# Performance work log

Measured on AMD Instinct MI355X. Metric: run time of the kernel, lower is better.

Reference implementation:

```python
import jax, jax.numpy as jnp
import numpy as np

WINDOW = 60
DEPTH = 3
HIDDEN = 256
LN_EPS = 1e-5


def _lyndon_indices(d):
    # Lyndon words over alphabet {0..d-1}, lengths 2 and 3, lexicographic order
    # (signatory mode='words' extracts expanded-logsig coefficients at Lyndon words).
    i2 = np.array([(i, j) for i in range(d) for j in range(d) if (i, j) < (j, i)], dtype=np.int32)
    i3 = np.array([(i, j, k) for i in range(d) for j in range(d) for k in range(d)
                   if (i, j, k) < (j, k, i) and (i, j, k) < (k, i, j)], dtype=np.int32)
    return i2, i3


def _logsig_features(x):
    # x: [b, s, c] -> logsignature of time-augmented sliding windows: [b*s, sig_channels]
    b, s, c = x.shape
    d = c + 1
    # replicate-padded sliding windows via clipped gather (matches F.pad replicate + unfold)
    pos = jnp.clip(jnp.arange(s)[:, None] + jnp.arange(WINDOW)[None, :] - (WINDOW - 1), 0, s - 1)
    windows = x[:, pos, :]                                   # [b, s, W, c]
    t = jnp.linspace(0.0, 1.0, WINDOW, dtype=x.dtype)        # time augmentation channel
    t_b = jnp.broadcast_to(t[None, None, :, None], (b, s, WINDOW, 1))
    aug = jnp.concatenate([t_b, windows], axis=-1).reshape(b * s, WINDOW, d)
    N = b * s
    # basepoint=True: prepend zero point -> increments include the first point itself
    inc = jnp.diff(aug, axis=1, prepend=jnp.zeros((N, 1, d), aug.dtype))  # [N, W, d]
    inc_t = jnp.transpose(inc, (1, 0, 2))                    # [W, N, d]

    def chen_step(carry, v):
        S1, S2, S3 = carry
        vv = jnp.einsum('ni,nj->nij', v, v)
        vvv = jnp.einsum('nij,nk->nijk', vv, v)
        nS3 = S3 + jnp.einsum('nij,nk->nijk', S2, v) \
                 + 0.5 * jnp.einsum('ni,njk->nijk', S1, vv) + vvv / 6.0
        nS2 = S2 + jnp.einsum('ni,nj->nij', S1, v) + 0.5 * vv
        nS1 = S1 + v
        return (nS1, nS2, nS3), None

    init = (jnp.zeros((N, d), x.dtype), jnp.zeros((N, d, d), x.dtype), jnp.zeros((N, d, d, d), x.dtype))
    (S1, S2, S3), _ = jax.lax.scan(chen_step, init, inc_t)
    # log in truncated tensor algebra: log(1+x) = x - x^2/2 + x^3/3
    L1 = S1
    L2 = S2 - 0.5 * jnp.einsum('ni,nj->nij', S1, S1)
    L3 = (S3 - 0.5 * (jnp.einsum('ni,njk->nijk', S1, S2) + jnp.einsum('nij,nk->nijk', S2, S1))
          + jnp.einsum('ni,nj,nk->nijk', S1, S1, S1) / 3.0)
    i2, i3 = _lyndon_indices(d)
    f2 = L2[:, i2[:, 0], i2[:, 1]]
    f3 = L3[:, i3[:, 0], i3[:, 1], i3[:, 2]]
    return jnp.concatenate([L1, f2, f3], axis=-1)            # [N, sig_channels]


def setup_inputs() -> dict:
    key = jax.random.key(0)
    ks = jax.random.split(key, 5)
    b, s, c = 8, 2048, 8
    d = c + 1
    sig_channels = d + (d * d - d) // 2 + (d ** 3 - d) // 3  # 285 for d=9
    h2 = 2 * HIDDEN
    x = jax.random.normal(ks[0], (b, s, c), dtype=jnp.float32)
    w1 = jax.random.normal(ks[1], (sig_channels, h2), dtype=jnp.float32) / np.sqrt(sig_channels)
    b1 = jnp.zeros((h2,), jnp.float32)
    ln_g = jnp.ones((h2,), jnp.float32)
    ln_b = jnp.zeros((h2,), jnp.float32)
    w2 = jax.random.normal(ks[2], (h2, HIDDEN), dtype=jnp.float32) / np.sqrt(h2)
    b2 = jnp.zeros((HIDDEN,), jnp.float32)
    return {"x": x, "w1": w1, "b1": b1, "ln_g": ln_g, "ln_b": ln_b, "w2": w2, "b2": b2}


def reference(x, w1, b1, ln_g, ln_b, w2, b2):
    b, s, _ = x.shape
    feats = _logsig_features(x)                              # [b*s, sig_channels]
    h = jax.nn.gelu(feats @ w1 + b1, approximate=False)      # torch default GELU (erf)
    mu = jnp.mean(h, axis=-1, keepdims=True)
    var = jnp.var(h, axis=-1, keepdims=True)
    h = (h - mu) / jnp.sqrt(var + LN_EPS) * ln_g + ln_b      # LayerNorm; Dropout is eval no-op
    out = h @ w2 + b2
    return out.reshape(b, s, -1)
```

## Files before the change

### kernel.cpp

```cpp
#include <hip/hip_runtime.h>
#include <hip/hip_bf16.h>
#include <cstdint>
#include <cstddef>

typedef short short8 __attribute__((ext_vector_type(8)));
typedef float f32x4 __attribute__((ext_vector_type(4)));
typedef float f32x2 __attribute__((ext_vector_type(2)));

#define NS    2048
#define KPAD  288
#define H2    512
#define HID   256
#define WPB   7
#define SBLK  293

#define MFMA(a,b,c) __builtin_amdgcn_mfma_f32_16x16x32_bf16((a),(b),(c),0,0,0)

__device__ __forceinline__ void gl2lds16(const void* g, void* l) {
    __builtin_amdgcn_global_load_lds(
        (const __attribute__((address_space(1))) void*)g,
        (__attribute__((address_space(3))) void*)l, 16, 0, 0);
}
__device__ __forceinline__ float geluf(float x) {
    return 0.5f * x * (1.0f + erff(x * 0.70710678118654752f));
}
__device__ __forceinline__ f32x4 shfl4(f32x4 v, int d) {
    f32x4 r;
    r[0] = __shfl_xor(v[0], d); r[1] = __shfl_xor(v[1], d);
    r[2] = __shfl_xor(v[2], d); r[3] = __shfl_xor(v[3], d);
    return r;
}

struct Tbl3 { short col[729]; };
static constexpr Tbl3 make_tbl3() {
    Tbl3 t{};
    for (int x = 0; x < 729; ++x) t.col[x] = -1;
    int r = 0;
    for (int i = 0; i < 9; ++i)
        for (int j = 0; j < 9; ++j)
            for (int k = 0; k < 9; ++k) {
                bool lt1 = (i < j) || (i == j && (j < k || (j == k && k < i)));
                bool lt2 = (i < k) || (i == k && (j < i || (j == i && k < j)));
                if (lt1 && lt2) { t.col[(i*9+j)*9+k] = (short)(45 + r); ++r; }
            }
    return t;
}
static constexpr Tbl3 TBL3 = make_tbl3();

#define SIG_STEP(VA_,VB_,VC_) { \
    const float hh = 0.5f * S1i + vi * (1.0f/6.0f); \
    const float ra = S2ra + hh * (VA_); \
    const float rb = S2rb + hh * (VB_); \
    const float rc = S2rc + hh * (VC_); \
    const f32x2 ra2 = {ra, ra}, rb2 = {rb, rb}, rc2 = {rc, rc}; \
    S3sa += ra * v0; S3pa0 += ra2*vp0; S3pa1 += ra2*vp1; S3pa2 += ra2*vp2; S3pa3 += ra2*vp3; \
    S3sb += rb * v0; S3pb0 += rb2*vp0; S3pb1 += rb2*vp1; S3pb2 += rb2*vp2; S3pb3 += rb2*vp3; \
    S3sc += rc * v0; S3pc0 += rc2*vp0; S3pc1 += rc2*vp1; S3pc2 += rc2*vp2; S3pc3 += rc2*vp3; \
    const float aa = S1i + 0.5f * vi; \
    S2ra += aa * (VA_); S2rb += aa * (VB_); S2rc += aa * (VC_); \
    S1i += vi; }

#define SIG_MAIN(VA_,VB_,VC_) { \
    { const float* xr = &X[(g0 - lo) * 8]; \
      const float4 e0 = *(const float4*)xr; \
      const float4 e1 = *(const float4*)(xr + 4); \
      const float rs = xr[ioff]; \
      const float v0 = 0.0f; \
      const f32x2 vp0 = {e0.x, e0.y}, vp1 = {e0.z, e0.w}, vp2 = {e1.x, e1.y}, vp3 = {e1.z, e1.w}; \
      const float vi = (ci == 0) ? 0.0f : rs; \
      SIG_STEP(VA_,VB_,VC_) } \
    const float* pd = &PD[(sm59 + 1 - lo + 59) * 8]; \
    float4 d0 = *(const float4*)pd; \
    float4 d1 = *(const float4*)(pd + 4); \
    float rn = pd[ioff]; \
    _Pragma("unroll 2") \
    for (int j = 1; j < 60; ++j) { \
      const float4 e0 = d0; const float4 e1 = d1; const float rs = rn; \
      pd += 8; \
      d0 = *(const float4*)pd; d1 = *(const float4*)(pd + 4); rn = pd[ioff]; \
      const float v0 = DT; \
      const f32x2 vp0 = {e0.x, e0.y}, vp1 = {e0.z, e0.w}, vp2 = {e1.x, e1.y}, vp3 = {e1.z, e1.w}; \
      const float vi = (ci == 0) ? DT : rs; \
      SIG_STEP(VA_,VB_,VC_) \
    } }

#define SIG_ST(RA,RB,RC) \
    if (act) { \
        if ((RA) == 0) S1buf[widx * 9 + ci] = S1i; \
        float* sb = &S2buf[widx * 81 + ci * 9]; \
        sb[RA] = S2ra; sb[RB] = S2rb; sb[RC] = S2rc; \
    }

#define S3EL0(SL) S3s##SL
#define S3EL1(SL) S3p##SL##0[0]
#define S3EL2(SL) S3p##SL##0[1]
#define S3EL3(SL) S3p##SL##1[0]
#define S3EL4(SL) S3p##SL##1[1]
#define S3EL5(SL) S3p##SL##2[0]
#define S3EL6(SL) S3p##SL##2[1]
#define S3EL7(SL) S3p##SL##3[0]
#define S3EL8(SL) S3p##SL##3[1]

#define SIG_E2(SL,J2) if (ci < (J2)) { \
    const float val2 = S2r##SL - 0.5f * S1i * s1v##J2; \
    const int col2 = 9 + ci*8 - (ci*(ci-1))/2 + ((J2) - ci - 1); \
    frow[col2] = __float2bfloat16(val2); }

#define SIG_E3(SL,R,K) { const int col3 = TBL3.col[tb + (R)*9 + (K)]; \
    if (col3 >= 0) { \
        const float val3 = S3EL##K(SL) \
            - 0.5f * (S1i * S2w[(R)*9+(K)] + S2r##SL * s1v##K) \
            + S1i * s1v##R * s1v##K * (1.0f/3.0f); \
        frow[col3] = __float2bfloat16(val3); } }

#define SIG_E3R(SL,R) SIG_E3(SL,R,0) SIG_E3(SL,R,1) SIG_E3(SL,R,2) SIG_E3(SL,R,3) \
    SIG_E3(SL,R,4) SIG_E3(SL,R,5) SIG_E3(SL,R,6) SIG_E3(SL,R,7) SIG_E3(SL,R,8)

#define SIG_EMIT(RA,RB,RC) \
    if (act) { \
        if ((RA) == 0) { \
            frow[ci] = __float2bfloat16(S1i); \
            if (ci == 0) { \
                const __hip_bfloat16 z16 = __float2bfloat16(0.0f); \
                frow[285] = z16; frow[286] = z16; frow[287] = z16; \
            } \
        } \
        SIG_E2(a,RA) SIG_E2(b,RB) SIG_E2(c,RC) \
        SIG_E3R(a,RA) SIG_E3R(b,RB) SIG_E3R(c,RC) \
    }

__global__ __launch_bounds__(192) __attribute__((amdgpu_waves_per_eu(1, 6)))
void sig_kernel(const float* __restrict__ x, __hip_bfloat16* __restrict__ feats) {
    __shared__ __align__(16) float X[66 * 8];
    __shared__ __align__(16) float PD[126 * 8];
    __shared__ float S2buf[WPB * 81];
    __shared__ float S1buf[WPB * 9];

    const int blk = blockIdx.x;
    const int b   = blk / SBLK;
    const int s0  = (blk % SBLK) * WPB;
    const int lo  = (s0 - 59 > 0) ? (s0 - 59) : 0;
    const int hi  = (s0 + WPB - 1 < NS - 1) ? (s0 + WPB - 1) : (NS - 1);
    const int nrow = hi - lo + 1;
    const int tid = threadIdx.x;

    {
        const float4* src = (const float4*)(x + ((size_t)b * NS + lo) * 8);
        float4* X4 = (float4*)X;
        const int n4 = nrow * 2;
        for (int t = tid; t < n4; t += 192) X4[t] = src[t];
    }
    __syncthreads();
    {
        const float4* X4 = (const float4*)X;
        float4* PD4 = (float4*)PD;
        for (int t = tid; t < 252; t += 192) {
            const int p = t >> 1;
            const int r = p - 59;
            float4 dv = {0.f, 0.f, 0.f, 0.f};
            if (r > 0 && r < nrow) {
                const float4 a = X4[t - 118], bb = X4[t - 120];
                dv.x = a.x - bb.x; dv.y = a.y - bb.y; dv.z = a.z - bb.z; dv.w = a.w - bb.w;
            }
            PD4[t] = dv;
        }
    }
    __syncthreads();

    const int t3    = tid >> 6;
    const int lt    = tid & 63;
    const int widx0 = lt / 9;
    const int ci    = lt - widx0 * 9;
    const bool act  = (lt < 63) && (s0 + widx0 < NS);
    const int widx  = (widx0 < WPB - 1) ? widx0 : WPB - 1;
    int s = s0 + widx; if (s > NS - 1) s = NS - 1;

    float S3sa=0.f, S3sb=0.f, S3sc=0.f;
    f32x2 S3pa0={0.f,0.f},S3pa1={0.f,0.f},S3pa2={0.f,0.f},S3pa3={0.f,0.f};
    f32x2 S3pb0={0.f,0.f},S3pb1={0.f,0.f},S3pb2={0.f,0.f},S3pb3={0.f,0.f};
    f32x2 S3pc0={0.f,0.f},S3pc1={0.f,0.f},S3pc2={0.f,0.f},S3pc3={0.f,0.f};
    float S2ra=0.f, S2rb=0.f, S2rc=0.f;
    float S1i = 0.f;
    const int ioff = (ci > 0) ? (ci - 1) : 0;
    const int sm59 = s - 59;
    const int g0   = (sm59 > 0) ? sm59 : 0;
    const float DT = 1.0f / 59.0f;

    if (t3 == 0)      { SIG_MAIN(v0,   e0.x, e0.y) }
    else if (t3 == 1) { SIG_MAIN(e0.z, e0.w, e1.x) }
    else              { SIG_MAIN(e1.y, e1.z, e1.w) }

    if (t3 == 0)      { SIG_ST(0,1,2) }
    else if (t3 == 1) { SIG_ST(3,4,5) }
    else              { SIG_ST(6,7,8) }
    __syncthreads();

    const float* s1p = &S1buf[widx * 9];
    const float s1v0=s1p[0], s1v1=s1p[1], s1v2=s1p[2], s1v3=s1p[3], s1v4=s1p[4];
    const float s1v5=s1p[5], s1v6=s1p[6], s1v7=s1p[7], s1v8=s1p[8];
    const float* S2w = &S2buf[widx * 81];
    const int tb = ci * 81;
    __hip_bfloat16* frow = feats + (size_t)(b * NS + s) * KPAD;

    if (t3 == 0)      { SIG_EMIT(0,1,2) }
    else if (t3 == 1) { SIG_EMIT(3,4,5) }
    else              { SIG_EMIT(6,7,8) }
}

__global__ void convert_w1(const float* __restrict__ w1, __hip_bfloat16* __restrict__ w1T) {
    const int n = blockIdx.x;
    const int k = threadIdx.x;
    const float v = (k < 285) ? w1[(size_t)k * H2 + n] : 0.0f;
    w1T[(size_t)n * KPAD + k] = __float2bfloat16(v);
}
__global__ void convert_w2g(const float* __restrict__ w2, const float* __restrict__ lng,
                            const float* __restrict__ lnb, const float* __restrict__ b2,
                            __hip_bfloat16* __restrict__ w2g, float* __restrict__ gw,
                            float* __restrict__ cvec) {
    const int n = blockIdx.x, k = threadIdx.x;
    const float wv = w2[(size_t)k * HID + n];
    const float a = lng[k] * wv;
    const float c = lnb[k] * wv;
    w2g[(size_t)n * H2 + k] = __float2bfloat16(a);
    float ra = a, rc = c;
#pragma unroll
    for (int d = 1; d < 64; d <<= 1) { ra += __shfl_xor(ra, d); rc += __shfl_xor(rc, d); }
    __shared__ float r1[8], r2[8];
    const int wv_ = k >> 6, ln = k & 63;
    if (ln == 0) { r1[wv_] = ra; r2[wv_] = rc; }
    __syncthreads();
    if (k == 0) {
        float sa = 0.f, sc = 0.f;
#pragma unroll
        for (int i = 0; i < 8; ++i) { sa += r1[i]; sc += r2[i]; }
        gw[n] = sa; cvec[n] = sc + b2[n];
    }
}

#define GDECL \
    f32x4 acc00={0,0,0,0},acc01={0,0,0,0},acc02={0,0,0,0},acc03={0,0,0,0}; \
    f32x4 acc10={0,0,0,0},acc11={0,0,0,0},acc12={0,0,0,0},acc13={0,0,0,0}; \
    f32x4 acc20={0,0,0,0},acc21={0,0,0,0},acc22={0,0,0,0},acc23={0,0,0,0}; \
    f32x4 acc30={0,0,0,0},acc31={0,0,0,0},acc32={0,0,0,0},acc33={0,0,0,0};

#define GMROW(mf) { const short8 av = *(const short8*)(abase + (mf)*512); \
    acc##mf##0 = MFMA(av, b0v, acc##mf##0); acc##mf##1 = MFMA(av, b1v, acc##mf##1); \
    acc##mf##2 = MFMA(av, b2v, acc##mf##2); acc##mf##3 = MFMA(av, b3v, acc##mf##3); }

#define GEMM_KLOOP(APTR, BPTR, KD, KSTEPS) \
    _Pragma("unroll 1") \
    for (int kt = 0; kt < (KSTEPS); ++kt) { \
        const int K0 = kt * 32; \
        { int c = tid; \
          gl2lds16((APTR) + (size_t)(m0 + (c>>2))*(KD) + K0 + (c&3)*8, (char*)ldsA + (c & ~63)*16); \
          gl2lds16((BPTR) + (size_t)(n0 + (c>>2))*(KD) + K0 + (c&3)*8, (char*)ldsB + (c & ~63)*16); \
          c = tid + 256; \
          gl2lds16((APTR) + (size_t)(m0 + (c>>2))*(KD) + K0 + (c&3)*8, (char*)ldsA + (c & ~63)*16); \
          gl2lds16((BPTR) + (size_t)(n0 + (c>>2))*(KD) + K0 + (c&3)*8, (char*)ldsB + (c & ~63)*16); } \
        __syncthreads(); \
        const __hip_bfloat16* abase = ldsA + (mh + l16)*32 + quad*8; \
        const __hip_bfloat16* bbase = ldsB + (nh + l16)*32 + quad*8; \
        const short8 b0v = *(const short8*)(bbase); \
        const short8 b1v = *(const short8*)(bbase + 512); \
        const short8 b2v = *(const short8*)(bbase + 1024); \
        const short8 b3v = *(const short8*)(bbase + 1536); \
        GMROW(0) GMROW(1) GMROW(2) GMROW(3) \
        __syncthreads(); \
    }

#define G1EP(mf,nf) { \
    const int colv = n0 + nh + (nf)*16 + l16; \
    const float bv = bias[colv]; \
    f32x4 e; \
    e[0] = geluf(acc##mf##nf[0] + bv); e[1] = geluf(acc##mf##nf[1] + bv); \
    e[2] = geluf(acc##mf##nf[2] + bv); e[3] = geluf(acc##mf##nf[3] + bv); \
    const int rrow = m0 + mh + (mf)*16 + quad*4; \
    h1[(size_t)(rrow+0)*H2 + colv] = __float2bfloat16(e[0]); \
    h1[(size_t)(rrow+1)*H2 + colv] = __float2bfloat16(e[1]); \
    h1[(size_t)(rrow+2)*H2 + colv] = __float2bfloat16(e[2]); \
    h1[(size_t)(rrow+3)*H2 + colv] = __float2bfloat16(e[3]); \
    sum##mf += e; sq##mf += e*e; }

#define G1RED(mf) { \
    f32x4 s = sum##mf, q = sq##mf; \
    s += shfl4(s,1); q += shfl4(q,1); s += shfl4(s,2); q += shfl4(q,2); \
    s += shfl4(s,4); q += shfl4(q,4); s += shfl4(s,8); q += shfl4(q,8); \
    if (l16 == 0) { const int rrow = m0 + mh + (mf)*16 + quad*4; \
        atomicAdd(&stats[2*(rrow+0)],   s[0]); atomicAdd(&stats[2*(rrow+0)+1], q[0]); \
        atomicAdd(&stats[2*(rrow+1)],   s[1]); atomicAdd(&stats[2*(rrow+1)+1], q[1]); \
        atomicAdd(&stats[2*(rrow+2)],   s[2]); atomicAdd(&stats[2*(rrow+2)+1], q[2]); \
        atomicAdd(&stats[2*(rrow+3)],   s[3]); atomicAdd(&stats[2*(rrow+3)+1], q[3]); } }

__global__ __launch_bounds__(256) __attribute__((amdgpu_waves_per_eu(1, 4)))
void gemm1_kernel(const __hip_bfloat16* __restrict__ feats,
                  const __hip_bfloat16* __restrict__ w1T,
                  const float* __restrict__ bias,
                  __hip_bfloat16* __restrict__ h1,
                  float* __restrict__ stats) {
    __shared__ __align__(16) __hip_bfloat16 ldsA[128 * 32];
    __shared__ __align__(16) __hip_bfloat16 ldsB[128 * 32];
    const int tid  = threadIdx.x;
    const int wave = tid >> 6;
    const int lane = tid & 63;
    const int quad = lane >> 4;
    const int l16  = lane & 15;
    const int mh   = (wave >> 1) * 64;
    const int nh   = (wave & 1) * 64;
    const int m0   = blockIdx.x * 128;
    const int n0   = blockIdx.y * 128;
    GDECL
    GEMM_KLOOP(feats, w1T, KPAD, 9)
    f32x4 sum0={0,0,0,0},sum1={0,0,0,0},sum2={0,0,0,0},sum3={0,0,0,0};
    f32x4 sq0={0,0,0,0},sq1={0,0,0,0},sq2={0,0,0,0},sq3={0,0,0,0};
    G1EP(0,0) G1EP(0,1) G1EP(0,2) G1EP(0,3)
    G1EP(1,0) G1EP(1,1) G1EP(1,2) G1EP(1,3)
    G1EP(2,0) G1EP(2,1) G1EP(2,2) G1EP(2,3)
    G1EP(3,0) G1EP(3,1) G1EP(3,2) G1EP(3,3)
    G1RED(0) G1RED(1) G1RED(2) G1RED(3)
}

#define STATR(r) { const float su = stats[2*(rrow+(r))]; const float qu = stats[2*(rrow+(r))+1]; \
    const float m_ = su * (1.0f/512.0f); const float v_ = qu * (1.0f/512.0f) - m_*m_; \
    muv[r] = m_; rsv[r] = rsqrtf(v_ + 1e-5f); }

#define G2C(mf,nf) { const int colv = n0 + nh + (nf)*16 + l16; \
    const float g_ = gw[colv], c_ = cvec[colv]; \
    out[(size_t)(rrow+0)*HID + colv] = rsv[0]*(acc##mf##nf[0] - muv[0]*g_) + c_; \
    out[(size_t)(rrow+1)*HID + colv] = rsv[1]*(acc##mf##nf[1] - muv[1]*g_) + c_; \
    out[(size_t)(rrow+2)*HID + colv] = rsv[2]*(acc##mf##nf[2] - muv[2]*g_) + c_; \
    out[(size_t)(rrow+3)*HID + colv] = rsv[3]*(acc##mf##nf[3] - muv[3]*g_) + c_; }

#define G2EP(mf) { const int rrow = m0 + mh + (mf)*16 + quad*4; \
    f32x4 muv, rsv; \
    STATR(0) STATR(1) STATR(2) STATR(3) \
    G2C(mf,0) G2C(mf,1) G2C(mf,2) G2C(mf,3) }

__global__ __launch_bounds__(256) __attribute__((amdgpu_waves_per_eu(1, 4)))
void gemm2_kernel(const __hip_bfloat16* __restrict__ h1,
                  const __hip_bfloat16* __restrict__ w2g,
                  const float* __restrict__ stats,
                  const float* __restrict__ gw,
                  const float* __restrict__ cvec,
                  float* __restrict__ out) {
    __shared__ __align__(16) __hip_bfloat16 ldsA[128 * 32];
    __shared__ __align__(16) __hip_bfloat16 ldsB[128 * 32];
    const int tid  = threadIdx.x;
    const int wave = tid >> 6;
    const int lane = tid & 63;
    const int quad = lane >> 4;
    const int l16  = lane & 15;
    const int mh   = (wave >> 1) * 64;
    const int nh   = (wave & 1) * 64;
    const int m0   = blockIdx.x * 128;
    const int n0   = blockIdx.y * 128;
    GDECL
    GEMM_KLOOP(h1, w2g, H2, 16)
    G2EP(0) G2EP(1) G2EP(2) G2EP(3)
}

extern "C" void kernel_launch(void* const* d_in, const int* in_sizes, int n_in,
                              void* d_out, int out_size, void* d_ws, size_t ws_size,
                              hipStream_t stream) {
    const float* x   = (const float*)d_in[0];
    const float* w1  = (const float*)d_in[1];
    const float* b1  = (const float*)d_in[2];
    const float* lng = (const float*)d_in[3];
    const float* lnb = (const float*)d_in[4];
    const float* w2  = (const float*)d_in[5];
    const float* b2  = (const float*)d_in[6];
    float* out = (float*)d_out;

    char* ws = (char*)d_ws;
    __hip_bfloat16* feats = (__hip_bfloat16*)(ws);
    __hip_bfloat16* h1    = (__hip_bfloat16*)(ws + 9437184);
    __hip_bfloat16* w1T   = (__hip_bfloat16*)(ws + 26214400);
    __hip_bfloat16* w2g   = (__hip_bfloat16*)(ws + 26509312);
    float*          gw    = (float*)(ws + 26771456);
    float*          cvec  = (float*)(ws + 26775552);
    float*          stats = (float*)(ws + 26779648);

    hipMemsetAsync(stats, 0, 16384 * 2 * sizeof(float), stream);
    convert_w1<<<dim3(512), dim3(288), 0, stream>>>(w1, w1T);
    convert_w2g<<<dim3(256), dim3(512), 0, stream>>>(w2, lng, lnb, b2, w2g, gw, cvec);
    sig_kernel<<<dim3(8 * SBLK), dim3(192), 0, stream>>>(x, feats);
    gemm1_kernel<<<dim3(128, 4), dim3(256), 0, stream>>>(feats, w1T, b1, h1, stats);
    gemm2_kernel<<<dim3(128, 2), dim3(256), 0, stream>>>(h1, w2g, stats, gw, cvec, out);
}
```

Baseline: 163.7 us.

## Fuse LayerNorm into GEMM1 with full-row tiles and direct-register MFMA loads

GEMM1 now gives each block 64 full rows of all 512 hidden columns, so the LayerNorm statistics can be reduced in shared memory and applied in the epilogue. This removes the global atomic stats buffer, its memset, and the folded gamma/beta weights used by GEMM2. Both GEMMs drop LDS staging and load MFMA operands straight from global memory into registers. GEMM2 becomes a plain GEMM plus bias with smaller 32-row tiles. The trade-off is more register pressure from 16 accumulators per wave and no LDS reuse of the B tiles, which now depends on L1/L2 caching.

New measurement: 204.7 us. 25.1% more time.

```diff
diff --git a/kernel.cpp b/kernel.cpp
--- a/kernel.cpp
+++ b/kernel.cpp
@@ -16,11 +16,6 @@
 
 #define MFMA(a,b,c) __builtin_amdgcn_mfma_f32_16x16x32_bf16((a),(b),(c),0,0,0)
 
-__device__ __forceinline__ void gl2lds16(const void* g, void* l) {
-    __builtin_amdgcn_global_load_lds(
-        (const __attribute__((address_space(1))) void*)g,
-        (__attribute__((address_space(3))) void*)l, 16, 0, 0);
-}
 __device__ __forceinline__ float geluf(float x) {
     return 0.5f * x * (1.0f + erff(x * 0.70710678118654752f));
 }
@@ -213,149 +208,131 @@
     const float v = (k < 285) ? w1[(size_t)k * H2 + n] : 0.0f;
     w1T[(size_t)n * KPAD + k] = __float2bfloat16(v);
 }
-__global__ void convert_w2g(const float* __restrict__ w2, const float* __restrict__ lng,
-                            const float* __restrict__ lnb, const float* __restrict__ b2,
-                            __hip_bfloat16* __restrict__ w2g, float* __restrict__ gw,
-                            float* __restrict__ cvec) {
-    const int n = blockIdx.x, k = threadIdx.x;
-    const float wv = w2[(size_t)k * HID + n];
-    const float a = lng[k] * wv;
-    const float c = lnb[k] * wv;
-    w2g[(size_t)n * H2 + k] = __float2bfloat16(a);
-    float ra = a, rc = c;
-#pragma unroll
-    for (int d = 1; d < 64; d <<= 1) { ra += __shfl_xor(ra, d); rc += __shfl_xor(rc, d); }
-    __shared__ float r1[8], r2[8];
-    const int wv_ = k >> 6, ln = k & 63;
-    if (ln == 0) { r1[wv_] = ra; r2[wv_] = rc; }
-    __syncthreads();
-    if (k == 0) {
-        float sa = 0.f, sc = 0.f;
-#pragma unroll
-        for (int i = 0; i < 8; ++i) { sa += r1[i]; sc += r2[i]; }
-        gw[n] = sa; cvec[n] = sc + b2[n];
-    }
-}
-
-#define GDECL \
-    f32x4 acc00={0,0,0,0},acc01={0,0,0,0},acc02={0,0,0,0},acc03={0,0,0,0}; \
-    f32x4 acc10={0,0,0,0},acc11={0,0,0,0},acc12={0,0,0,0},acc13={0,0,0,0}; \
-    f32x4 acc20={0,0,0,0},acc21={0,0,0,0},acc22={0,0,0,0},acc23={0,0,0,0}; \
-    f32x4 acc30={0,0,0,0},acc31={0,0,0,0},acc32={0,0,0,0},acc33={0,0,0,0};
-
-#define GMROW(mf) { const short8 av = *(const short8*)(abase + (mf)*512); \
-    acc##mf##0 = MFMA(av, b0v, acc##mf##0); acc##mf##1 = MFMA(av, b1v, acc##mf##1); \
-    acc##mf##2 = MFMA(av, b2v, acc##mf##2); acc##mf##3 = MFMA(av, b3v, acc##mf##3); }
-
-#define GEMM_KLOOP(APTR, BPTR, KD, KSTEPS) \
-    _Pragma("unroll 1") \
-    for (int kt = 0; kt < (KSTEPS); ++kt) { \
-        const int K0 = kt * 32; \
-        { int c = tid; \
-          gl2lds16((APTR) + (size_t)(m0 + (c>>2))*(KD) + K0 + (c&3)*8, (char*)ldsA + (c & ~63)*16); \
-          gl2lds16((BPTR) + (size_t)(n0 + (c>>2))*(KD) + K0 + (c&3)*8, (char*)ldsB + (c & ~63)*16); \
-          c = tid + 256; \
-          gl2lds16((APTR) + (size_t)(m0 + (c>>2))*(KD) + K0 + (c&3)*8, (char*)ldsA + (c & ~63)*16); \
-          gl2lds16((BPTR) + (size_t)(n0 + (c>>2))*(KD) + K0 + (c&3)*8, (char*)ldsB + (c & ~63)*16); } \
-        __syncthreads(); \
-        const __hip_bfloat16* abase = ldsA + (mh + l16)*32 + quad*8; \
-        const __hip_bfloat16* bbase = ldsB + (nh + l16)*32 + quad*8; \
-        const short8 b0v = *(const short8*)(bbase); \
-        const short8 b1v = *(const short8*)(bbase + 512); \
-        const short8 b2v = *(const short8*)(bbase + 1024); \
-        const short8 b3v = *(const short8*)(bbase + 1536); \
-        GMROW(0) GMROW(1) GMROW(2) GMROW(3) \
-        __syncthreads(); \
-    }
-
-#define G1EP(mf,nf) { \
-    const int colv = n0 + nh + (nf)*16 + l16; \
-    const float bv = bias[colv]; \
-    f32x4 e; \
-    e[0] = geluf(acc##mf##nf[0] + bv); e[1] = geluf(acc##mf##nf[1] + bv); \
-    e[2] = geluf(acc##mf##nf[2] + bv); e[3] = geluf(acc##mf##nf[3] + bv); \
-    const int rrow = m0 + mh + (mf)*16 + quad*4; \
-    h1[(size_t)(rrow+0)*H2 + colv] = __float2bfloat16(e[0]); \
-    h1[(size_t)(rrow+1)*H2 + colv] = __float2bfloat16(e[1]); \
-    h1[(size_t)(rrow+2)*H2 + colv] = __float2bfloat16(e[2]); \
-    h1[(size_t)(rrow+3)*H2 + colv] = __float2bfloat16(e[3]); \
-    sum##mf += e; sq##mf += e*e; }
-
-#define G1RED(mf) { \
-    f32x4 s = sum##mf, q = sq##mf; \
-    s += shfl4(s,1); q += shfl4(q,1); s += shfl4(s,2); q += shfl4(q,2); \
-    s += shfl4(s,4); q += shfl4(q,4); s += shfl4(s,8); q += shfl4(q,8); \
-    if (l16 == 0) { const int rrow = m0 + mh + (mf)*16 + quad*4; \
-        atomicAdd(&stats[2*(rrow+0)],   s[0]); atomicAdd(&stats[2*(rrow+0)+1], q[0]); \
-        atomicAdd(&stats[2*(rrow+1)],   s[1]); atomicAdd(&stats[2*(rrow+1)+1], q[1]); \
-        atomicAdd(&stats[2*(rrow+2)],   s[2]); atomicAdd(&stats[2*(rrow+2)+1], q[2]); \
-        atomicAdd(&stats[2*(rrow+3)],   s[3]); atomicAdd(&stats[2*(rrow+3)+1], q[3]); } }
-
-__global__ __launch_bounds__(256) __attribute__((amdgpu_waves_per_eu(1, 4)))
+__global__ void convert_w2(const float* __restrict__ w2, __hip_bfloat16* __restrict__ w2T) {
+    const int n = blockIdx.x;
+    const int k = threadIdx.x;
+    w2T[(size_t)n * H2 + k] = __float2bfloat16(w2[(size_t)k * HID + n]);
+}
+
+#define REP16(M) M(0) M(1) M(2) M(3) M(4) M(5) M(6) M(7) M(8) M(9) M(10) M(11) M(12) M(13) M(14) M(15)
+#define REP8(M)  M(0) M(1) M(2) M(3) M(4) M(5) M(6) M(7)
+
+#define G1_DECL(nf) f32x4 acc##nf = {0.f,0.f,0.f,0.f};
+#define G1_LD(nf)   const short8 bv##nf = *(const short8*)(brow + (nf)*16*KPAD + ko);
+#define G1_FM(nf)   acc##nf = MFMA(av, bv##nf, acc##nf);
+#define G1_BIAS(nf) const float bias##nf = b1[wc*256 + (nf)*16 + l16];
+#define G1_GELU(nf) { acc##nf[0]=geluf(acc##nf[0]+bias##nf); acc##nf[1]=geluf(acc##nf[1]+bias##nf); \
+                      acc##nf[2]=geluf(acc##nf[2]+bias##nf); acc##nf[3]=geluf(acc##nf[3]+bias##nf); }
+#define G1_OUT(nf) { const int col = wc*256 + (nf)*16 + l16; \
+    const float g_ = lng[col], b_ = lnb[col]; \
+    hp[0*H2 + col] = __float2bfloat16((acc##nf[0]-mu0)*rs0*g_ + b_); \
+    hp[1*H2 + col] = __float2bfloat16((acc##nf[1]-mu1)*rs1*g_ + b_); \
+    hp[2*H2 + col] = __float2bfloat16((acc##nf[2]-mu2)*rs2*g_ + b_); \
+    hp[3*H2 + col] = __float2bfloat16((acc##nf[3]-mu3)*rs3*g_ + b_); }
+
+__global__ __launch_bounds__(512) __attribute__((amdgpu_waves_per_eu(1, 4)))
 void gemm1_kernel(const __hip_bfloat16* __restrict__ feats,
                   const __hip_bfloat16* __restrict__ w1T,
-                  const float* __restrict__ bias,
-                  __hip_bfloat16* __restrict__ h1,
-                  float* __restrict__ stats) {
-    __shared__ __align__(16) __hip_bfloat16 ldsA[128 * 32];
-    __shared__ __align__(16) __hip_bfloat16 ldsB[128 * 32];
+                  const float* __restrict__ b1,
+                  const float* __restrict__ lng,
+                  const float* __restrict__ lnb,
+                  __hip_bfloat16* __restrict__ h1) {
+    __shared__ float lnpart[2][64][2];
+    __shared__ float lnstat[64][2];
     const int tid  = threadIdx.x;
     const int wave = tid >> 6;
     const int lane = tid & 63;
     const int quad = lane >> 4;
     const int l16  = lane & 15;
-    const int mh   = (wave >> 1) * 64;
-    const int nh   = (wave & 1) * 64;
-    const int m0   = blockIdx.x * 128;
-    const int n0   = blockIdx.y * 128;
-    GDECL
-    GEMM_KLOOP(feats, w1T, KPAD, 9)
-    f32x4 sum0={0,0,0,0},sum1={0,0,0,0},sum2={0,0,0,0},sum3={0,0,0,0};
-    f32x4 sq0={0,0,0,0},sq1={0,0,0,0},sq2={0,0,0,0},sq3={0,0,0,0};
-    G1EP(0,0) G1EP(0,1) G1EP(0,2) G1EP(0,3)
-    G1EP(1,0) G1EP(1,1) G1EP(1,2) G1EP(1,3)
-    G1EP(2,0) G1EP(2,1) G1EP(2,2) G1EP(2,3)
-    G1EP(3,0) G1EP(3,1) G1EP(3,2) G1EP(3,3)
-    G1RED(0) G1RED(1) G1RED(2) G1RED(3)
-}
-
-#define STATR(r) { const float su = stats[2*(rrow+(r))]; const float qu = stats[2*(rrow+(r))+1]; \
-    const float m_ = su * (1.0f/512.0f); const float v_ = qu * (1.0f/512.0f) - m_*m_; \
-    muv[r] = m_; rsv[r] = rsqrtf(v_ + 1e-5f); }
-
-#define G2C(mf,nf) { const int colv = n0 + nh + (nf)*16 + l16; \
-    const float g_ = gw[colv], c_ = cvec[colv]; \
-    out[(size_t)(rrow+0)*HID + colv] = rsv[0]*(acc##mf##nf[0] - muv[0]*g_) + c_; \
-    out[(size_t)(rrow+1)*HID + colv] = rsv[1]*(acc##mf##nf[1] - muv[1]*g_) + c_; \
-    out[(size_t)(rrow+2)*HID + colv] = rsv[2]*(acc##mf##nf[2] - muv[2]*g_) + c_; \
-    out[(size_t)(rrow+3)*HID + colv] = rsv[3]*(acc##mf##nf[3] - muv[3]*g_) + c_; }
-
-#define G2EP(mf) { const int rrow = m0 + mh + (mf)*16 + quad*4; \
-    f32x4 muv, rsv; \
-    STATR(0) STATR(1) STATR(2) STATR(3) \
-    G2C(mf,0) G2C(mf,1) G2C(mf,2) G2C(mf,3) }
+    const int wr   = wave >> 1;
+    const int wc   = wave & 1;
+    const int m0   = blockIdx.x * 64;
+
+    const __hip_bfloat16* arow = feats + (size_t)(m0 + wr*16 + l16) * KPAD + quad*8;
+    const __hip_bfloat16* brow = w1T   + (size_t)(wc*256 + l16) * KPAD + quad*8;
+
+    REP16(G1_DECL)
+#pragma unroll 1
+    for (int kt = 0; kt < 9; ++kt) {
+        const int ko = kt * 32;
+        const short8 av = *(const short8*)(arow + ko);
+        REP16(G1_LD)
+        REP16(G1_FM)
+    }
+
+    REP16(G1_BIAS)
+    REP16(G1_GELU)
+
+    f32x4 s = acc0+acc1+acc2+acc3+acc4+acc5+acc6+acc7+acc8+acc9+acc10+acc11+acc12+acc13+acc14+acc15;
+    f32x4 q = acc0*acc0+acc1*acc1+acc2*acc2+acc3*acc3+acc4*acc4+acc5*acc5+acc6*acc6+acc7*acc7
+            + acc8*acc8+acc9*acc9+acc10*acc10+acc11*acc11+acc12*acc12+acc13*acc13+acc14*acc14+acc15*acc15;
+    s += shfl4(s,1); q += shfl4(q,1);
+    s += shfl4(s,2); q += shfl4(q,2);
+    s += shfl4(s,4); q += shfl4(q,4);
+    s += shfl4(s,8); q += shfl4(q,8);
+    if (l16 == 0) {
+#pragma unroll
+        for (int r = 0; r < 4; ++r) {
+            lnpart[wc][wr*16 + quad*4 + r][0] = s[r];
+            lnpart[wc][wr*16 + quad*4 + r][1] = q[r];
+        }
+    }
+    __syncthreads();
+    if (tid < 64) {
+        const float su = lnpart[0][tid][0] + lnpart[1][tid][0];
+        const float qu = lnpart[0][tid][1] + lnpart[1][tid][1];
+        const float mu  = su * (1.0f / 512.0f);
+        const float var = qu * (1.0f / 512.0f) - mu * mu;
+        lnstat[tid][0] = mu;
+        lnstat[tid][1] = rsqrtf(var + 1e-5f);
+    }
+    __syncthreads();
+    const int rb = wr*16 + quad*4;
+    const float mu0 = lnstat[rb+0][0], rs0 = lnstat[rb+0][1];
+    const float mu1 = lnstat[rb+1][0], rs1 = lnstat[rb+1][1];
+    const float mu2 = lnstat[rb+2][0], rs2 = lnstat[rb+2][1];
+    const float mu3 = lnstat[rb+3][0], rs3 = lnstat[rb+3][1];
+    __hip_bfloat16* hp = h1 + (size_t)(m0 + rb) * H2;
+    REP16(G1_OUT)
+}
+
+#define G2_DECL(nf) f32x4 acc##nf = {0.f,0.f,0.f,0.f};
+#define G2_LD(nf)   const short8 bv##nf = *(const short8*)(brow + (nf)*16*H2 + ko);
+#define G2_FM(nf)   acc##nf = MFMA(av, bv##nf, acc##nf);
+#define G2_OUT(nf) { const int col = wc*128 + (nf)*16 + l16; \
+    const float b_ = b2[col]; \
+    op[0*HID + col] = acc##nf[0] + b_; \
+    op[1*HID + col] = acc##nf[1] + b_; \
+    op[2*HID + col] = acc##nf[2] + b_; \
+    op[3*HID + col] = acc##nf[3] + b_; }
 
 __global__ __launch_bounds__(256) __attribute__((amdgpu_waves_per_eu(1, 4)))
 void gemm2_kernel(const __hip_bfloat16* __restrict__ h1,
-                  const __hip_bfloat16* __restrict__ w2g,
-                  const float* __restrict__ stats,
-                  const float* __restrict__ gw,
-                  const float* __restrict__ cvec,
+                  const __hip_bfloat16* __restrict__ w2T,
+                  const float* __restrict__ b2,
                   float* __restrict__ out) {
-    __shared__ __align__(16) __hip_bfloat16 ldsA[128 * 32];
-    __shared__ __align__(16) __hip_bfloat16 ldsB[128 * 32];
     const int tid  = threadIdx.x;
     const int wave = tid >> 6;
     const int lane = tid & 63;
     const int quad = lane >> 4;
     const int l16  = lane & 15;
-    const int mh   = (wave >> 1) * 64;
-    const int nh   = (wave & 1) * 64;
-    const int m0   = blockIdx.x * 128;
-    const int n0   = blockIdx.y * 128;
-    GDECL
-    GEMM_KLOOP(h1, w2g, H2, 16)
-    G2EP(0) G2EP(1) G2EP(2) G2EP(3)
+    const int wr   = wave >> 1;
+    const int wc   = wave & 1;
+    const int m0   = blockIdx.x * 32;
+
+    const __hip_bfloat16* arow = h1  + (size_t)(m0 + wr*16 + l16) * H2 + quad*8;
+    const __hip_bfloat16* brow = w2T + (size_t)(wc*128 + l16) * H2 + quad*8;
+
+    REP8(G2_DECL)
+#pragma unroll 1
+    for (int kt = 0; kt < 16; ++kt) {
+        const int ko = kt * 32;
+        const short8 av = *(const short8*)(arow + ko);
+        REP8(G2_LD)
+        REP8(G2_FM)
+    }
+    float* op = out + (size_t)(m0 + wr*16 + quad*4) * HID;
+    REP8(G2_OUT)
 }
 
 extern "C" void kernel_launch(void* const* d_in, const int* in_sizes, int n_in,
@@ -374,15 +351,11 @@
     __hip_bfloat16* feats = (__hip_bfloat16*)(ws);
     __hip_bfloat16* h1    = (__hip_bfloat16*)(ws + 9437184);
     __hip_bfloat16* w1T   = (__hip_bfloat16*)(ws + 26214400);
-    __hip_bfloat16* w2g   = (__hip_bfloat16*)(ws + 26509312);
-    float*          gw    = (float*)(ws + 26771456);
-    float*          cvec  = (float*)(ws + 26775552);
-    float*          stats = (float*)(ws + 26779648);
-
-    hipMemsetAsync(stats, 0, 16384 * 2 * sizeof(float), stream);
+    __hip_bfloat16* w2T   = (__hip_bfloat16*)(ws + 26509312);
+
     convert_w1<<<dim3(512), dim3(288), 0, stream>>>(w1, w1T);
-    convert_w2g<<<dim3(256), dim3(512), 0, stream>>>(w2, lng, lnb, b2, w2g, gw, cvec);
+    convert_w2<<<dim3(256), dim3(512), 0, stream>>>(w2, w2T);
     sig_kernel<<<dim3(8 * SBLK), dim3(192), 0, stream>>>(x, feats);
-    gemm1_kernel<<<dim3(128, 4), dim3(256), 0, stream>>>(feats, w1T, b1, h1, stats);
-    gemm2_kernel<<<dim3(128, 2), dim3(256), 0, stream>>>(h1, w2g, stats, gw, cvec, out);
-}
+    gemm1_kernel<<<dim3(16384 / 64), dim3(512), 0, stream>>>(feats, w1T, b1, lng, lnb, h1);
+    gemm2_kernel<<<dim3(16384 / 32), dim3(256), 0, stream>>>(h1, w2T, b2, out);
+}
```

## Keep full-K weight slice in LDS, stream A from global, drop atomics

Applied to the files above, without the earlier changes.

Both GEMMs are retiled so each block loads its whole-K slice of the weight matrix into padded LDS once. Each wave then streams its 32 A rows straight from global memory with no per-k-step barriers, and the grid grows to 128x8 blocks. LayerNorm row statistics are written as per-column-block partials into a 16-slot layout and summed in gemm2, replacing the atomics and the memset. The trade-off is less A reuse per block, more redundant A traffic across column blocks, and unpipelined global loads feeding the MFMAs.

New measurement: 167.1 us. +2.1%, slower.

```diff
diff --git a/kernel.cpp b/kernel.cpp
--- a/kernel.cpp
+++ b/kernel.cpp
@@ -13,14 +13,11 @@
 #define HID   256
 #define WPB   7
 #define SBLK  293
+#define KLDS1 296
+#define KLDS2 520
 
 #define MFMA(a,b,c) __builtin_amdgcn_mfma_f32_16x16x32_bf16((a),(b),(c),0,0,0)
 
-__device__ __forceinline__ void gl2lds16(const void* g, void* l) {
-    __builtin_amdgcn_global_load_lds(
-        (const __attribute__((address_space(1))) void*)g,
-        (__attribute__((address_space(3))) void*)l, 16, 0, 0);
-}
 __device__ __forceinline__ float geluf(float x) {
     return 0.5f * x * (1.0f + erff(x * 0.70710678118654752f));
 }
@@ -237,103 +234,97 @@
     }
 }
 
-#define GDECL \
-    f32x4 acc00={0,0,0,0},acc01={0,0,0,0},acc02={0,0,0,0},acc03={0,0,0,0}; \
-    f32x4 acc10={0,0,0,0},acc11={0,0,0,0},acc12={0,0,0,0},acc13={0,0,0,0}; \
-    f32x4 acc20={0,0,0,0},acc21={0,0,0,0},acc22={0,0,0,0},acc23={0,0,0,0}; \
-    f32x4 acc30={0,0,0,0},acc31={0,0,0,0},acc32={0,0,0,0},acc33={0,0,0,0};
-
-#define GMROW(mf) { const short8 av = *(const short8*)(abase + (mf)*512); \
-    acc##mf##0 = MFMA(av, b0v, acc##mf##0); acc##mf##1 = MFMA(av, b1v, acc##mf##1); \
-    acc##mf##2 = MFMA(av, b2v, acc##mf##2); acc##mf##3 = MFMA(av, b3v, acc##mf##3); }
-
-#define GEMM_KLOOP(APTR, BPTR, KD, KSTEPS) \
-    _Pragma("unroll 1") \
-    for (int kt = 0; kt < (KSTEPS); ++kt) { \
-        const int K0 = kt * 32; \
-        { int c = tid; \
-          gl2lds16((APTR) + (size_t)(m0 + (c>>2))*(KD) + K0 + (c&3)*8, (char*)ldsA + (c & ~63)*16); \
-          gl2lds16((BPTR) + (size_t)(n0 + (c>>2))*(KD) + K0 + (c&3)*8, (char*)ldsB + (c & ~63)*16); \
-          c = tid + 256; \
-          gl2lds16((APTR) + (size_t)(m0 + (c>>2))*(KD) + K0 + (c&3)*8, (char*)ldsA + (c & ~63)*16); \
-          gl2lds16((BPTR) + (size_t)(n0 + (c>>2))*(KD) + K0 + (c&3)*8, (char*)ldsB + (c & ~63)*16); } \
-        __syncthreads(); \
-        const __hip_bfloat16* abase = ldsA + (mh + l16)*32 + quad*8; \
-        const __hip_bfloat16* bbase = ldsB + (nh + l16)*32 + quad*8; \
-        const short8 b0v = *(const short8*)(bbase); \
-        const short8 b1v = *(const short8*)(bbase + 512); \
-        const short8 b2v = *(const short8*)(bbase + 1024); \
-        const short8 b3v = *(const short8*)(bbase + 1536); \
-        GMROW(0) GMROW(1) GMROW(2) GMROW(3) \
-        __syncthreads(); \
-    }
-
-#define G1EP(mf,nf) { \
-    const int colv = n0 + nh + (nf)*16 + l16; \
-    const float bv = bias[colv]; \
-    f32x4 e; \
-    e[0] = geluf(acc##mf##nf[0] + bv); e[1] = geluf(acc##mf##nf[1] + bv); \
-    e[2] = geluf(acc##mf##nf[2] + bv); e[3] = geluf(acc##mf##nf[3] + bv); \
-    const int rrow = m0 + mh + (mf)*16 + quad*4; \
-    h1[(size_t)(rrow+0)*H2 + colv] = __float2bfloat16(e[0]); \
-    h1[(size_t)(rrow+1)*H2 + colv] = __float2bfloat16(e[1]); \
-    h1[(size_t)(rrow+2)*H2 + colv] = __float2bfloat16(e[2]); \
-    h1[(size_t)(rrow+3)*H2 + colv] = __float2bfloat16(e[3]); \
-    sum##mf += e; sq##mf += e*e; }
-
-#define G1RED(mf) { \
-    f32x4 s = sum##mf, q = sq##mf; \
-    s += shfl4(s,1); q += shfl4(q,1); s += shfl4(s,2); q += shfl4(q,2); \
-    s += shfl4(s,4); q += shfl4(q,4); s += shfl4(s,8); q += shfl4(q,8); \
-    if (l16 == 0) { const int rrow = m0 + mh + (mf)*16 + quad*4; \
-        atomicAdd(&stats[2*(rrow+0)],   s[0]); atomicAdd(&stats[2*(rrow+0)+1], q[0]); \
-        atomicAdd(&stats[2*(rrow+1)],   s[1]); atomicAdd(&stats[2*(rrow+1)+1], q[1]); \
-        atomicAdd(&stats[2*(rrow+2)],   s[2]); atomicAdd(&stats[2*(rrow+2)+1], q[2]); \
-        atomicAdd(&stats[2*(rrow+3)],   s[3]); atomicAdd(&stats[2*(rrow+3)+1], q[3]); } }
-
 __global__ __launch_bounds__(256) __attribute__((amdgpu_waves_per_eu(1, 4)))
 void gemm1_kernel(const __hip_bfloat16* __restrict__ feats,
                   const __hip_bfloat16* __restrict__ w1T,
-                  const float* __restrict__ bias,
+                  const float* __restrict__ b1,
                   __hip_bfloat16* __restrict__ h1,
                   float* __restrict__ stats) {
-    __shared__ __align__(16) __hip_bfloat16 ldsA[128 * 32];
-    __shared__ __align__(16) __hip_bfloat16 ldsB[128 * 32];
+    __shared__ __align__(16) __hip_bfloat16 ldsB[64 * KLDS1];
     const int tid  = threadIdx.x;
     const int wave = tid >> 6;
     const int lane = tid & 63;
     const int quad = lane >> 4;
     const int l16  = lane & 15;
-    const int mh   = (wave >> 1) * 64;
-    const int nh   = (wave & 1) * 64;
-    const int m0   = blockIdx.x * 128;
-    const int n0   = blockIdx.y * 128;
-    GDECL
-    GEMM_KLOOP(feats, w1T, KPAD, 9)
-    f32x4 sum0={0,0,0,0},sum1={0,0,0,0},sum2={0,0,0,0},sum3={0,0,0,0};
-    f32x4 sq0={0,0,0,0},sq1={0,0,0,0},sq2={0,0,0,0},sq3={0,0,0,0};
-    G1EP(0,0) G1EP(0,1) G1EP(0,2) G1EP(0,3)
-    G1EP(1,0) G1EP(1,1) G1EP(1,2) G1EP(1,3)
-    G1EP(2,0) G1EP(2,1) G1EP(2,2) G1EP(2,3)
-    G1EP(3,0) G1EP(3,1) G1EP(3,2) G1EP(3,3)
-    G1RED(0) G1RED(1) G1RED(2) G1RED(3)
-}
-
-#define STATR(r) { const float su = stats[2*(rrow+(r))]; const float qu = stats[2*(rrow+(r))+1]; \
-    const float m_ = su * (1.0f/512.0f); const float v_ = qu * (1.0f/512.0f) - m_*m_; \
-    muv[r] = m_; rsv[r] = rsqrtf(v_ + 1e-5f); }
-
-#define G2C(mf,nf) { const int colv = n0 + nh + (nf)*16 + l16; \
-    const float g_ = gw[colv], c_ = cvec[colv]; \
-    out[(size_t)(rrow+0)*HID + colv] = rsv[0]*(acc##mf##nf[0] - muv[0]*g_) + c_; \
-    out[(size_t)(rrow+1)*HID + colv] = rsv[1]*(acc##mf##nf[1] - muv[1]*g_) + c_; \
-    out[(size_t)(rrow+2)*HID + colv] = rsv[2]*(acc##mf##nf[2] - muv[2]*g_) + c_; \
-    out[(size_t)(rrow+3)*HID + colv] = rsv[3]*(acc##mf##nf[3] - muv[3]*g_) + c_; }
-
-#define G2EP(mf) { const int rrow = m0 + mh + (mf)*16 + quad*4; \
-    f32x4 muv, rsv; \
-    STATR(0) STATR(1) STATR(2) STATR(3) \
-    G2C(mf,0) G2C(mf,1) G2C(mf,2) G2C(mf,3) }
+    const int m0   = blockIdx.x * 128 + wave * 32;
+    const int n0   = blockIdx.y * 64;
+    const int nb   = blockIdx.y;
+
+    for (int c = tid; c < 64 * 36; c += 256) {
+        const int n = c / 36, k8 = c - n * 36;
+        *(short8*)(ldsB + n * KLDS1 + k8 * 8) =
+            *(const short8*)(w1T + (size_t)(n0 + n) * KPAD + k8 * 8);
+    }
+    __syncthreads();
+
+    const __hip_bfloat16* a0 = feats + (size_t)(m0 + l16) * KPAD + quad * 8;
+    const __hip_bfloat16* a1 = feats + (size_t)(m0 + 16 + l16) * KPAD + quad * 8;
+    const __hip_bfloat16* bb = ldsB + l16 * KLDS1 + quad * 8;
+
+    f32x4 acc00={0,0,0,0},acc01={0,0,0,0},acc02={0,0,0,0},acc03={0,0,0,0};
+    f32x4 acc10={0,0,0,0},acc11={0,0,0,0},acc12={0,0,0,0},acc13={0,0,0,0};
+#pragma unroll 1
+    for (int kt = 0; kt < 9; ++kt) {
+        const int ko = kt * 32;
+        const short8 av0 = *(const short8*)(a0 + ko);
+        const short8 av1 = *(const short8*)(a1 + ko);
+        const short8 bv0 = *(const short8*)(bb + ko);
+        const short8 bv1 = *(const short8*)(bb + 16 * KLDS1 + ko);
+        const short8 bv2 = *(const short8*)(bb + 32 * KLDS1 + ko);
+        const short8 bv3 = *(const short8*)(bb + 48 * KLDS1 + ko);
+        acc00 = MFMA(av0, bv0, acc00); acc01 = MFMA(av0, bv1, acc01);
+        acc02 = MFMA(av0, bv2, acc02); acc03 = MFMA(av0, bv3, acc03);
+        acc10 = MFMA(av1, bv0, acc10); acc11 = MFMA(av1, bv1, acc11);
+        acc12 = MFMA(av1, bv2, acc12); acc13 = MFMA(av1, bv3, acc13);
+    }
+
+    const float bias0 = b1[n0 +  0 + l16];
+    const float bias1 = b1[n0 + 16 + l16];
+    const float bias2 = b1[n0 + 32 + l16];
+    const float bias3 = b1[n0 + 48 + l16];
+#define G1G(A,B) { A[0]=geluf(A[0]+B); A[1]=geluf(A[1]+B); A[2]=geluf(A[2]+B); A[3]=geluf(A[3]+B); }
+    G1G(acc00,bias0) G1G(acc01,bias1) G1G(acc02,bias2) G1G(acc03,bias3)
+    G1G(acc10,bias0) G1G(acc11,bias1) G1G(acc12,bias2) G1G(acc13,bias3)
+#undef G1G
+
+    f32x4 s0 = acc00 + acc01 + acc02 + acc03;
+    f32x4 q0 = acc00*acc00 + acc01*acc01 + acc02*acc02 + acc03*acc03;
+    f32x4 s1 = acc10 + acc11 + acc12 + acc13;
+    f32x4 q1 = acc10*acc10 + acc11*acc11 + acc12*acc12 + acc13*acc13;
+    s0 += shfl4(s0,1); q0 += shfl4(q0,1); s1 += shfl4(s1,1); q1 += shfl4(q1,1);
+    s0 += shfl4(s0,2); q0 += shfl4(q0,2); s1 += shfl4(s1,2); q1 += shfl4(q1,2);
+    s0 += shfl4(s0,4); q0 += shfl4(q0,4); s1 += shfl4(s1,4); q1 += shfl4(q1,4);
+    s0 += shfl4(s0,8); q0 += shfl4(q0,8); s1 += shfl4(s1,8); q1 += shfl4(q1,8);
+    if (l16 == 0) {
+#pragma unroll
+        for (int r = 0; r < 4; ++r) {
+            const int r0 = m0 + quad * 4 + r;
+            stats[r0 * 16 + nb] = s0[r]; stats[r0 * 16 + 8 + nb] = q0[r];
+            const int r1 = r0 + 16;
+            stats[r1 * 16 + nb] = s1[r]; stats[r1 * 16 + 8 + nb] = q1[r];
+        }
+    }
+
+    {
+        __hip_bfloat16* hp = h1 + (size_t)(m0 + quad * 4) * H2;
+        const int c0 = n0 + l16;
+#pragma unroll
+        for (int r = 0; r < 4; ++r) {
+            hp[(size_t)r * H2 + c0     ] = __float2bfloat16(acc00[r]);
+            hp[(size_t)r * H2 + c0 + 16] = __float2bfloat16(acc01[r]);
+            hp[(size_t)r * H2 + c0 + 32] = __float2bfloat16(acc02[r]);
+            hp[(size_t)r * H2 + c0 + 48] = __float2bfloat16(acc03[r]);
+        }
+        __hip_bfloat16* hp2 = hp + (size_t)16 * H2;
+#pragma unroll
+        for (int r = 0; r < 4; ++r) {
+            hp2[(size_t)r * H2 + c0     ] = __float2bfloat16(acc10[r]);
+            hp2[(size_t)r * H2 + c0 + 16] = __float2bfloat16(acc11[r]);
+            hp2[(size_t)r * H2 + c0 + 32] = __float2bfloat16(acc12[r]);
+            hp2[(size_t)r * H2 + c0 + 48] = __float2bfloat16(acc13[r]);
+        }
+    }
+}
 
 __global__ __launch_bounds__(256) __attribute__((amdgpu_waves_per_eu(1, 4)))
 void gemm2_kernel(const __hip_bfloat16* __restrict__ h1,
@@ -342,20 +333,59 @@
                   const float* __restrict__ gw,
                   const float* __restrict__ cvec,
                   float* __restrict__ out) {
-    __shared__ __align__(16) __hip_bfloat16 ldsA[128 * 32];
-    __shared__ __align__(16) __hip_bfloat16 ldsB[128 * 32];
+    __shared__ __align__(16) __hip_bfloat16 ldsB[32 * KLDS2];
     const int tid  = threadIdx.x;
     const int wave = tid >> 6;
     const int lane = tid & 63;
     const int quad = lane >> 4;
     const int l16  = lane & 15;
-    const int mh   = (wave >> 1) * 64;
-    const int nh   = (wave & 1) * 64;
-    const int m0   = blockIdx.x * 128;
-    const int n0   = blockIdx.y * 128;
-    GDECL
-    GEMM_KLOOP(h1, w2g, H2, 16)
-    G2EP(0) G2EP(1) G2EP(2) G2EP(3)
+    const int m0   = blockIdx.x * 128 + wave * 32;
+    const int n0   = blockIdx.y * 32;
+
+    for (int c = tid; c < 32 * 64; c += 256) {
+        const int n = c >> 6, k8 = c & 63;
+        *(short8*)(ldsB + n * KLDS2 + k8 * 8) =
+            *(const short8*)(w2g + (size_t)(n0 + n) * H2 + k8 * 8);
+    }
+    __syncthreads();
+
+    const __hip_bfloat16* a0 = h1 + (size_t)(m0 + l16) * H2 + quad * 8;
+    const __hip_bfloat16* a1 = h1 + (size_t)(m0 + 16 + l16) * H2 + quad * 8;
+    const __hip_bfloat16* bb = ldsB + l16 * KLDS2 + quad * 8;
+
+    f32x4 acc00={0,0,0,0},acc01={0,0,0,0},acc10={0,0,0,0},acc11={0,0,0,0};
+#pragma unroll 1
+    for (int kt = 0; kt < 16; ++kt) {
+        const int ko = kt * 32;
+        const short8 av0 = *(const short8*)(a0 + ko);
+        const short8 av1 = *(const short8*)(a1 + ko);
+        const short8 bv0 = *(const short8*)(bb + ko);
+        const short8 bv1 = *(const short8*)(bb + 16 * KLDS2 + ko);
+        acc00 = MFMA(av0, bv0, acc00); acc01 = MFMA(av0, bv1, acc01);
+        acc10 = MFMA(av1, bv0, acc10); acc11 = MFMA(av1, bv1, acc11);
+    }
+
+    const int c0 = n0 + l16, c1 = c0 + 16;
+    const float gw0 = gw[c0], gw1 = gw[c1];
+    const float cv0 = cvec[c0], cv1 = cvec[c1];
+#define G2EP(mf) { \
+    const int rbase = m0 + (mf)*16 + quad*4; \
+    _Pragma("unroll") \
+    for (int r = 0; r < 4; ++r) { \
+        const int row = rbase + r; \
+        const float4 sA = *(const float4*)&stats[row*16]; \
+        const float4 sB = *(const float4*)&stats[row*16+4]; \
+        const float4 qA = *(const float4*)&stats[row*16+8]; \
+        const float4 qB = *(const float4*)&stats[row*16+12]; \
+        const float su = sA.x+sA.y+sA.z+sA.w + sB.x+sB.y+sB.z+sB.w; \
+        const float qu = qA.x+qA.y+qA.z+qA.w + qB.x+qB.y+qB.z+qB.w; \
+        const float mu = su * (1.0f/512.0f); \
+        const float rsv = rsqrtf(qu*(1.0f/512.0f) - mu*mu + 1e-5f); \
+        out[(size_t)row*HID + c0] = rsv*(acc##mf##0[r] - mu*gw0) + cv0; \
+        out[(size_t)row*HID + c1] = rsv*(acc##mf##1[r] - mu*gw1) + cv1; \
+    } }
+    G2EP(0) G2EP(1)
+#undef G2EP
 }
 
 extern "C" void kernel_launch(void* const* d_in, const int* in_sizes, int n_in,
@@ -379,10 +409,9 @@
     float*          cvec  = (float*)(ws + 26775552);
     float*          stats = (float*)(ws + 26779648);
 
-    hipMemsetAsync(stats, 0, 16384 * 2 * sizeof(float), stream);
     convert_w1<<<dim3(512), dim3(288), 0, stream>>>(w1, w1T);
     convert_w2g<<<dim3(256), dim3(512), 0, stream>>>(w2, lng, lnb, b2, w2g, gw, cvec);
     sig_kernel<<<dim3(8 * SBLK), dim3(192), 0, stream>>>(x, feats);
-    gemm1_kernel<<<dim3(128, 4), dim3(256), 0, stream>>>(feats, w1T, b1, h1, stats);
-    gemm2_kernel<<<dim3(128, 2), dim3(256), 0, stream>>>(h1, w2g, stats, gw, cvec, out);
-}
+    gemm1_kernel<<<dim3(128, 8), dim3(256), 0, stream>>>(feats, w1T, b1, h1, stats);
+    gemm2_kernel<<<dim3(128, 8), dim3(256), 0, stream>>>(h1, w2g, stats, gw, cvec, out);
+}
```
